# Optimization experiments

Hardware: AMD Instinct MI355X
Metric: run time of the kernel (lower is better)

Reference implementation:

```python
import jax, jax.numpy as jnp
import numpy as np

IN_F, HID, N_CLS = 128, 256, 2
N_NODES, N_EDGES = 50000, 800000


def setup_inputs() -> dict:
    key = jax.random.key(0)
    ks = jax.random.split(key, 8)
    x = jax.random.normal(ks[0], (N_NODES, IN_F), dtype=jnp.float32)
    edge_index = jax.random.randint(ks[1], (2, N_EDGES), 0, N_NODES, dtype=jnp.int64)
    # Linear params (torch nn.Linear: y = x @ W.T + b), uniform(-1/sqrt(fan_in), ..)
    def lin(k, out_f, in_f):
        k1, k2 = jax.random.split(k)
        bound = 1.0 / np.sqrt(in_f)
        W = jax.random.uniform(k1, (out_f, in_f), minval=-bound, maxval=bound, dtype=jnp.float32)
        b = jax.random.uniform(k2, (out_f,), minval=-bound, maxval=bound, dtype=jnp.float32)
        return W, b
    W1, b1 = lin(ks[2], HID, IN_F)
    W2, b2 = lin(ks[3], HID // 2, HID)
    W3, b3 = lin(ks[4], N_CLS, HID // 2)
    return {"x": x, "edge_index": edge_index, "n_nodes": N_NODES,
            "W1": W1, "b1": b1, "W2": W2, "b2": b2, "W3": W3, "b3": b3}


def _gcn_layer(x, row, col, deg_inv, n_nodes, W, b):
    # gather neighbor features, scatter-add into destinations, degree-normalize
    agg = jax.ops.segment_sum(x[row], col, num_segments=n_nodes)  # [N, F]
    agg = agg * deg_inv[:, None]
    return agg @ W.T + b


def reference(x, edge_index, n_nodes, W1, b1, W2, b2, W3, b3):
    row, col = edge_index[0], edge_index[1]
    deg = jax.ops.segment_sum(jnp.ones_like(col, dtype=x.dtype), col, num_segments=n_nodes)
    deg_inv = 1.0 / jnp.maximum(deg, 1.0)  # bincount().clamp(min=1)
    h = jax.nn.relu(_gcn_layer(x, row, col, deg_inv, n_nodes, W1, b1))
    # dropout is identity in eval mode
    h = jax.nn.relu(_gcn_layer(h, row, col, deg_inv, n_nodes, W2, b2))
    return h @ W3.T + b3  # [N, num_classes]
```

## Files before the change

kernel.cpp:

```cpp
#include <hip/hip_runtime.h>
#include <hip/hip_fp16.h>

#define IN_F 128
#define HID 256
#define HID2 128
#define MAXDEG 64

typedef __attribute__((ext_vector_type(8))) _Float16 f16x8;
typedef __attribute__((ext_vector_type(4))) float f32x4;

__global__ __launch_bounds__(256) void prep(
        const float* __restrict__ x,
        const float* __restrict__ W1, const float* __restrict__ W2,
        ushort* __restrict__ xh, ushort* __restrict__ w1h, ushort* __restrict__ w1l,
        ushort* __restrict__ w2h, ushort* __restrict__ w2l,
        int* __restrict__ fill, int N) {
    int gid = blockIdx.x * 256 + threadIdx.x, gsz = gridDim.x * 256;
    for (int i = gid; i < N; i += gsz) fill[i] = 0;
    int t8 = N * IN_F / 8;
    for (int i = gid; i < t8; i += gsz) {
        const float4* s4 = (const float4*)x + (size_t)i * 2;
        float4 f0 = s4[0], f1 = s4[1];
        uint4 o;
        o.x = __half_as_ushort(__float2half(f0.x)) | ((unsigned)__half_as_ushort(__float2half(f0.y)) << 16);
        o.y = __half_as_ushort(__float2half(f0.z)) | ((unsigned)__half_as_ushort(__float2half(f0.w)) << 16);
        o.z = __half_as_ushort(__float2half(f1.x)) | ((unsigned)__half_as_ushort(__float2half(f1.y)) << 16);
        o.w = __half_as_ushort(__float2half(f1.z)) | ((unsigned)__half_as_ushort(__float2half(f1.w)) << 16);
        ((uint4*)xh)[i] = o;
    }
    int nw = HID * IN_F + HID2 * HID;
    for (int i = gid; i < nw; i += gsz) {
        bool first = i < HID * IN_F;
        int j = first ? i : i - HID * IN_F;
        float f = first ? W1[j] : W2[j];
        __half h = __float2half(f);
        __half lo = __float2half(f - __half2float(h));
        if (first) { w1h[j] = __half_as_ushort(h); w1l[j] = __half_as_ushort(lo); }
        else       { w2h[j] = __half_as_ushort(h); w2l[j] = __half_as_ushort(lo); }
    }
}

__global__ void fill_csr(const int* __restrict__ row, const int* __restrict__ col,
                         int* __restrict__ fill, int* __restrict__ csr, int E) {
    int e = blockIdx.x * blockDim.x + threadIdx.x;
    if (e < E) {
        int c = col[e];
        int p = atomicAdd(&fill[c], 1);
        if (p < MAXDEG) csr[(size_t)c * MAXDEG + p] = row[e];
    }
}

__device__ __forceinline__ void add4h(float4& a, uint2 v) {
    float2 f0 = __half22float2(*(const __half2*)&v.x);
    float2 f1 = __half22float2(*(const __half2*)&v.y);
    a.x += f0.x; a.y += f0.y; a.z += f1.x; a.w += f1.y;
}

__global__ __launch_bounds__(256) void agg_gather(const ushort* __restrict__ xh,
                                                  const int* __restrict__ deg,
                                                  const int* __restrict__ csr,
                                                  ushort* __restrict__ outh, int N) {
    int w = threadIdx.x >> 6, lane = threadIdx.x & 63;
    int n = blockIdx.x * 4 + w;
    if (n >= N) return;
    int d = deg[n]; if (d > MAXDEG) d = MAXDEG;
    int s = n * MAXDEG, e = s + d;
    int half = lane >> 5, l = lane & 31;
    const uint2* xv = (const uint2*)xh;
    float4 a0 = {0,0,0,0}, a1 = {0,0,0,0}, a2 = {0,0,0,0}, a3 = {0,0,0,0};
    int i = s;
    for (; i + 7 < e; i += 8) {
        int s0 = csr[i + half], s1 = csr[i + 2 + half];
        int s2 = csr[i + 4 + half], s3 = csr[i + 6 + half];
        uint2 v0 = xv[(size_t)s0 * 32 + l];
        uint2 v1 = xv[(size_t)s1 * 32 + l];
        uint2 v2 = xv[(size_t)s2 * 32 + l];
        uint2 v3 = xv[(size_t)s3 * 32 + l];
        add4h(a0, v0); add4h(a1, v1); add4h(a2, v2); add4h(a3, v3);
    }
    for (; i + 1 < e; i += 2) {
        add4h(a0, xv[(size_t)csr[i + half] * 32 + l]);
    }
    if (i < e && half == 0) {
        add4h(a0, xv[(size_t)csr[i] * 32 + l]);
    }
    a0.x += a1.x + a2.x + a3.x; a0.y += a1.y + a2.y + a3.y;
    a0.z += a1.z + a2.z + a3.z; a0.w += a1.w + a2.w + a3.w;
    a0.x += __shfl_xor(a0.x, 32, 64);
    a0.y += __shfl_xor(a0.y, 32, 64);
    a0.z += __shfl_xor(a0.z, 32, 64);
    a0.w += __shfl_xor(a0.w, 32, 64);
    if (half == 0) {
        float dinv = 1.f / fmaxf((float)d, 1.f);
        uint2 o;
        o.x = __half_as_ushort(__float2half(a0.x * dinv)) |
              ((unsigned)__half_as_ushort(__float2half(a0.y * dinv)) << 16);
        o.y = __half_as_ushort(__float2half(a0.z * dinv)) |
              ((unsigned)__half_as_ushort(__float2half(a0.w * dinv)) << 16);
        ((uint2*)outh)[(size_t)n * 32 + l] = o;
    }
}

__global__ __launch_bounds__(256) void gemm_fused(const ushort* __restrict__ A,
                                                  const ushort* __restrict__ W1h,
                                                  const ushort* __restrict__ W1l,
                                                  const ushort* __restrict__ W2h,
                                                  const ushort* __restrict__ W2l,
                                                  const float* __restrict__ b1,
                                                  ushort* __restrict__ Z,
                                                  int M) {
    __shared__ _Float16 hs[64][HID + 8];
    int t = threadIdx.x;
    int wv = t >> 6, l = t & 63;
    int r = l & 15, q = l >> 4;
    int m0 = blockIdx.x * 64;
    const _Float16* Af = (const _Float16*)A;

    {
        int n0 = wv * 64;
        f16x8 WAh[4][4], WAl[4][4];
#pragma unroll
        for (int k4 = 0; k4 < 4; k4++) {
            int kf = k4 * 32 + q * 8;
#pragma unroll
            for (int j = 0; j < 4; j++) {
                size_t wo = (size_t)(n0 + 16 * j + r) * IN_F + kf;
                WAh[k4][j] = *(const f16x8*)((const _Float16*)W1h + wo);
                WAl[k4][j] = *(const f16x8*)((const _Float16*)W1l + wo);
            }
        }
        f32x4 acc[4][4];
#pragma unroll
        for (int i = 0; i < 4; i++)
#pragma unroll
            for (int j = 0; j < 4; j++) acc[i][j] = (f32x4){0.f, 0.f, 0.f, 0.f};
#pragma unroll
        for (int k4 = 0; k4 < 4; k4++) {
            int kf = k4 * 32 + q * 8;
            f16x8 a[4];
#pragma unroll
            for (int i = 0; i < 4; i++) {
                int m = m0 + 16 * i + r;
                if (m > M - 1) m = M - 1;
                a[i] = *(const f16x8*)(Af + (size_t)m * IN_F + kf);
            }
#pragma unroll
            for (int i = 0; i < 4; i++)
#pragma unroll
                for (int j = 0; j < 4; j++) {
                    acc[i][j] = __builtin_amdgcn_mfma_f32_16x16x32_f16(a[i], WAh[k4][j], acc[i][j], 0, 0, 0);
                    acc[i][j] = __builtin_amdgcn_mfma_f32_16x16x32_f16(a[i], WAl[k4][j], acc[i][j], 0, 0, 0);
                }
        }
#pragma unroll
        for (int j = 0; j < 4; j++) {
            int n = n0 + 16 * j + r;
            float bo = b1[n];
#pragma unroll
            for (int i = 0; i < 4; i++)
#pragma unroll
                for (int reg = 0; reg < 4; reg++) {
                    int mr = 16 * i + q * 4 + reg;
                    hs[mr][n] = (_Float16)fmaxf(acc[i][j][reg] + bo, 0.f);
                }
        }
    }
    __syncthreads();

    {
        int mb = (wv >> 1) * 32, n0 = (wv & 1) * 64;
        f32x4 acc[2][4];
#pragma unroll
        for (int i = 0; i < 2; i++)
#pragma unroll
            for (int j = 0; j < 4; j++) acc[i][j] = (f32x4){0.f, 0.f, 0.f, 0.f};
#pragma unroll
        for (int khalf = 0; khalf < 2; khalf++) {
            f16x8 WBh[4][4], WBl[4][4];
#pragma unroll
            for (int k4 = 0; k4 < 4; k4++) {
                int kf = khalf * 128 + k4 * 32 + q * 8;
#pragma unroll
                for (int j = 0; j < 4; j++) {
                    size_t wo = (size_t)(n0 + 16 * j + r) * HID + kf;
                    WBh[k4][j] = *(const f16x8*)((const _Float16*)W2h + wo);
                    WBl[k4][j] = *(const f16x8*)((const _Float16*)W2l + wo);
                }
            }
#pragma unroll
            for (int k4 = 0; k4 < 4; k4++) {
                int kf = khalf * 128 + k4 * 32 + q * 8;
                f16x8 a[2];
#pragma unroll
                for (int i = 0; i < 2; i++)
                    a[i] = *(const f16x8*)&hs[mb + 16 * i + r][kf];
#pragma unroll
                for (int i = 0; i < 2; i++)
#pragma unroll
                    for (int j = 0; j < 4; j++) {
                        acc[i][j] = __builtin_amdgcn_mfma_f32_16x16x32_f16(a[i], WBh[k4][j], acc[i][j], 0, 0, 0);
                        acc[i][j] = __builtin_amdgcn_mfma_f32_16x16x32_f16(a[i], WBl[k4][j], acc[i][j], 0, 0, 0);
                    }
            }
        }
#pragma unroll
        for (int i = 0; i < 2; i++)
#pragma unroll
            for (int reg = 0; reg < 4; reg++) {
                int m = m0 + mb + 16 * i + q * 4 + reg;
                if (m < M) {
#pragma unroll
                    for (int j = 0; j < 4; j++) {
                        int n = n0 + 16 * j + r;
                        Z[(size_t)m * HID2 + n] = __half_as_ushort(__float2half(acc[i][j][reg]));
                    }
                }
            }
    }
}

__global__ __launch_bounds__(256) void agg2_out(const ushort* __restrict__ zh,
                                                const int* __restrict__ deg,
                                                const int* __restrict__ csr,
                                                const float* __restrict__ b2,
                                                const float* __restrict__ W3,
                                                const float* __restrict__ b3,
                                                float* __restrict__ out, int N) {
    int w = threadIdx.x >> 6, lane = threadIdx.x & 63;
    int n = blockIdx.x * 4 + w;
    if (n >= N) return;
    int d = deg[n]; if (d > MAXDEG) d = MAXDEG;
    int s = n * MAXDEG, e = s + d;
    int half = lane >> 5, l = lane & 31;
    const uint2* zv = (const uint2*)zh;
    float4 a0 = {0,0,0,0}, a1 = {0,0,0,0}, a2 = {0,0,0,0}, a3 = {0,0,0,0};
    int i = s;
    for (; i + 7 < e; i += 8) {
        int s0 = csr[i + half], s1 = csr[i + 2 + half];
        int s2 = csr[i + 4 + half], s3 = csr[i + 6 + half];
        uint2 v0 = zv[(size_t)s0 * 32 + l];
        uint2 v1 = zv[(size_t)s1 * 32 + l];
        uint2 v2 = zv[(size_t)s2 * 32 + l];
        uint2 v3 = zv[(size_t)s3 * 32 + l];
        add4h(a0, v0); add4h(a1, v1); add4h(a2, v2); add4h(a3, v3);
    }
    for (; i + 1 < e; i += 2) {
        add4h(a0, zv[(size_t)csr[i + half] * 32 + l]);
    }
    if (i < e && half == 0) {
        add4h(a0, zv[(size_t)csr[i] * 32 + l]);
    }
    a0.x += a1.x + a2.x + a3.x; a0.y += a1.y + a2.y + a3.y;
    a0.z += a1.z + a2.z + a3.z; a0.w += a1.w + a2.w + a3.w;
    a0.x += __shfl_xor(a0.x, 32, 64);
    a0.y += __shfl_xor(a0.y, 32, 64);
    a0.z += __shfl_xor(a0.z, 32, 64);
    a0.w += __shfl_xor(a0.w, 32, 64);
    float dinv = 1.f / fmaxf((float)d, 1.f);
    float4 bb = ((const float4*)b2)[l];
    float4 ww = ((const float4*)W3)[half * 32 + l];
    float hx = fmaxf(a0.x * dinv + bb.x, 0.f);
    float hy = fmaxf(a0.y * dinv + bb.y, 0.f);
    float hz = fmaxf(a0.z * dinv + bb.z, 0.f);
    float hw = fmaxf(a0.w * dinv + bb.w, 0.f);
    float p = hx * ww.x + hy * ww.y + hz * ww.z + hw * ww.w;
#pragma unroll
    for (int d2 = 16; d2 > 0; d2 >>= 1) p += __shfl_xor(p, d2, 64);
    if (l == 0) out[(size_t)n * 2 + half] = p + b3[half];
}

extern "C" void kernel_launch(void* const* d_in, const int* in_sizes, int n_in,
                              void* d_out, int out_size, void* d_ws, size_t ws_size,
                              hipStream_t stream) {
    const float* x  = (const float*)d_in[0];
    const int*   ei = (const int*)d_in[1];
    const float* W1 = (const float*)d_in[3];
    const float* b1 = (const float*)d_in[4];
    const float* W2 = (const float*)d_in[5];
    const float* b2 = (const float*)d_in[6];
    const float* W3 = (const float*)d_in[7];
    const float* b3 = (const float*)d_in[8];
    float* out = (float*)d_out;

    int N = in_sizes[0] / IN_F;
    int E = in_sizes[1] / 2;
    const int* row = ei;
    const int* col = ei + E;

    char* base = (char*)d_ws;
    size_t off = 0;
    auto alloc = [&](size_t bytes) -> void* {
        off = (off + 255) & ~(size_t)255;
        void* p = base + off;
        off += bytes;
        return p;
    };
    int*    fill = (int*)alloc((size_t)N * 4);
    int*    csr  = (int*)alloc((size_t)N * MAXDEG * 4);
    ushort* xh   = (ushort*)alloc((size_t)N * IN_F * 2);
    ushort* f2h  = (ushort*)alloc((size_t)N * IN_F * 2);
    ushort* z2h  = (ushort*)alloc((size_t)N * HID2 * 2);
    ushort* w1h  = (ushort*)alloc(HID * IN_F * 2);
    ushort* w1l  = (ushort*)alloc(HID * IN_F * 2);
    ushort* w2h  = (ushort*)alloc(HID2 * HID * 2);
    ushort* w2l  = (ushort*)alloc(HID2 * HID * 2);

    int eb = (E + 255) / 256;
    prep<<<2048, 256, 0, stream>>>(x, W1, W2, xh, w1h, w1l, w2h, w2l, fill, N);
    fill_csr<<<eb, 256, 0, stream>>>(row, col, fill, csr, E);
    agg_gather<<<(N + 3) / 4, 256, 0, stream>>>(xh, fill, csr, f2h, N);
    gemm_fused<<<(N + 63) / 64, 256, 0, stream>>>(f2h, w1h, w1l, w2h, w2l, b1, z2h, N);
    agg2_out<<<(N + 3) / 4, 256, 0, stream>>>(z2h, fill, csr, b2, W3, b3, out, N);
}
```

Measured before the change: 250.5 us.

## Partition CSR build by destination and store neighbor indices as 16-bit

The CSR fill kernel now uses a fixed grid split into 8 destination-node partitions, interleaved by block index. Each block handles only edges whose destination lies in its partition, which aims to keep atomics and scattered writes within one cache domain. The cost is that every partition re-reads the col array. CSR entries are narrowed to ushort, halving CSR storage and gather index traffic, but this limits node count to 65536. The GEMM gets a two-blocks-per-CU launch bound and compiler memory barriers to shape its load scheduling.

```diff
diff --git a/kernel.cpp b/kernel.cpp
--- a/kernel.cpp
+++ b/kernel.cpp
@@ -5,6 +5,7 @@
 #define HID 256
 #define HID2 128
 #define MAXDEG 64
+#define NPART 8
 
 typedef __attribute__((ext_vector_type(8))) _Float16 f16x8;
 typedef __attribute__((ext_vector_type(4))) float f32x4;
@@ -40,13 +41,21 @@
     }
 }
 
-__global__ void fill_csr(const int* __restrict__ row, const int* __restrict__ col,
-                         int* __restrict__ fill, int* __restrict__ csr, int E) {
-    int e = blockIdx.x * blockDim.x + threadIdx.x;
-    if (e < E) {
+__global__ __launch_bounds__(256) void fill_csr(const int* __restrict__ row,
+                                                const int* __restrict__ col,
+                                                int* __restrict__ fill,
+                                                ushort* __restrict__ csr,
+                                                int E, int npp) {
+    int part = blockIdx.x & (NPART - 1);
+    int bi   = blockIdx.x >> 3;
+    int bpp  = gridDim.x >> 3;
+    int lo = part * npp, hi = lo + npp;
+    for (int e = bi * 256 + threadIdx.x; e < E; e += bpp * 256) {
         int c = col[e];
-        int p = atomicAdd(&fill[c], 1);
-        if (p < MAXDEG) csr[(size_t)c * MAXDEG + p] = row[e];
+        if (c >= lo && c < hi) {
+            int p = atomicAdd(&fill[c], 1);
+            if (p < MAXDEG) csr[(size_t)c * MAXDEG + p] = (ushort)row[e];
+        }
     }
 }
 
@@ -58,7 +67,7 @@
 
 __global__ __launch_bounds__(256) void agg_gather(const ushort* __restrict__ xh,
                                                   const int* __restrict__ deg,
-                                                  const int* __restrict__ csr,
+                                                  const ushort* __restrict__ csr,
                                                   ushort* __restrict__ outh, int N) {
     int w = threadIdx.x >> 6, lane = threadIdx.x & 63;
     int n = blockIdx.x * 4 + w;
@@ -101,7 +110,7 @@
     }
 }
 
-__global__ __launch_bounds__(256) void gemm_fused(const ushort* __restrict__ A,
+__global__ __launch_bounds__(256, 2) void gemm_fused(const ushort* __restrict__ A,
                                                   const ushort* __restrict__ W1h,
                                                   const ushort* __restrict__ W1l,
                                                   const ushort* __restrict__ W2h,
@@ -129,6 +138,7 @@
                 WAl[k4][j] = *(const f16x8*)((const _Float16*)W1l + wo);
             }
         }
+        asm volatile("" ::: "memory");
         f32x4 acc[4][4];
 #pragma unroll
         for (int i = 0; i < 4; i++)
@@ -187,6 +197,7 @@
                     WBl[k4][j] = *(const f16x8*)((const _Float16*)W2l + wo);
                 }
             }
+            asm volatile("" ::: "memory");
 #pragma unroll
             for (int k4 = 0; k4 < 4; k4++) {
                 int kf = khalf * 128 + k4 * 32 + q * 8;
@@ -221,7 +232,7 @@
 
 __global__ __launch_bounds__(256) void agg2_out(const ushort* __restrict__ zh,
                                                 const int* __restrict__ deg,
-                                                const int* __restrict__ csr,
+                                                const ushort* __restrict__ csr,
                                                 const float* __restrict__ b2,
                                                 const float* __restrict__ W3,
                                                 const float* __restrict__ b3,
@@ -296,7 +307,7 @@
         return p;
     };
     int*    fill = (int*)alloc((size_t)N * 4);
-    int*    csr  = (int*)alloc((size_t)N * MAXDEG * 4);
+    ushort* csr  = (ushort*)alloc((size_t)N * MAXDEG * 2);
     ushort* xh   = (ushort*)alloc((size_t)N * IN_F * 2);
     ushort* f2h  = (ushort*)alloc((size_t)N * IN_F * 2);
     ushort* z2h  = (ushort*)alloc((size_t)N * HID2 * 2);
@@ -305,9 +316,9 @@
     ushort* w2h  = (ushort*)alloc(HID2 * HID * 2);
     ushort* w2l  = (ushort*)alloc(HID2 * HID * 2);
 
-    int eb = (E + 255) / 256;
+    int npp = (N + NPART - 1) / NPART;
     prep<<<2048, 256, 0, stream>>>(x, W1, W2, xh, w1h, w1l, w2h, w2l, fill, N);
-    fill_csr<<<eb, 256, 0, stream>>>(row, col, fill, csr, E);
+    fill_csr<<<2048, 256, 0, stream>>>(row, col, fill, csr, E, npp);
     agg_gather<<<(N + 3) / 4, 256, 0, stream>>>(xh, fill, csr, f2h, N);
     gemm_fused<<<(N + 63) / 64, 256, 0, stream>>>(f2h, w1h, w1l, w2h, w2l, b1, z2h, N);
     agg2_out<<<(N + 3) / 4, 256, 0, stream>>>(z2h, fill, csr, b2, W3, b3, out, N);
```

Result: no change. 247.6 us (-1.2%).
